# Optimization experiments

Hardware: AMD Instinct MI355X
Metric: run time of the kernel (lower is better)

The kernel has to match this reference:

```python
import math
import jax, jax.numpy as jnp
import numpy as np

B, S, D, H, DH = 4, 1024, 768, 24, 64  # batch, seq, d_model, n_heads (12*2), d_head
DG = 1  # d_gate


def setup_inputs() -> dict:
    key = jax.random.key(0)
    ks = jax.random.split(key, 12)
    sc = 0.02
    return {
        "x": jax.random.normal(ks[0], (B, S, D), dtype=jnp.float32),
        "W_Q": jax.random.normal(ks[1], (H, D, DH), dtype=jnp.float32) * sc,
        "W_K": jax.random.normal(ks[2], (H, D, DH), dtype=jnp.float32) * sc,
        "W_V": jax.random.normal(ks[3], (H, D, DH), dtype=jnp.float32) * sc,
        "W_O": jax.random.normal(ks[4], (H, DH, D), dtype=jnp.float32) * sc,
        "b_Q": jax.random.normal(ks[5], (H, DH), dtype=jnp.float32) * sc,
        "b_K": jax.random.normal(ks[6], (H, DH), dtype=jnp.float32) * sc,
        "b_V": jax.random.normal(ks[7], (H, DH), dtype=jnp.float32) * sc,
        "W_gate_Q": jax.random.normal(ks[8], (H, D, DG), dtype=jnp.float32) * sc,
        "W_gate_K": jax.random.normal(ks[9], (H, D, DG), dtype=jnp.float32) * sc,
        "b_gate_Q": jnp.zeros((H, DG), dtype=jnp.float32),
        "b_gate_K": jnp.zeros((H, DG), dtype=jnp.float32),
    }


def reference(x, W_Q, W_K, W_V, W_O, b_Q, b_K, b_V,
              W_gate_Q, W_gate_K, b_gate_Q, b_gate_K):
    eps = 1e-12
    # F.normalize: L2 over d_model axis (dim=1 of W_V, dim=2 of W_O)
    W_Vn = W_V / jnp.maximum(jnp.linalg.norm(W_V, axis=1, keepdims=True), eps)
    W_On = W_O / jnp.maximum(jnp.linalg.norm(W_O, axis=2, keepdims=True), eps)

    q = jnp.einsum('hmd,bqm->bqhd', W_Q, x) + b_Q            # [B,S,H,DH]
    k = jnp.einsum('hmd,bkm->bkhd', W_K, x) + b_K
    v = jnp.einsum('hmd,bkm->bkhd', W_Vn, x) + b_V
    qg = jnp.einsum('hmg,bqm->bqhg', W_gate_Q, x) + b_gate_Q  # [B,S,H,1]
    kg = jnp.einsum('hmg,bkm->bkhg', W_gate_K, x) + b_gate_K

    scores = jnp.einsum('bqhd,bkhd->bhqk', q, k)              # [B,H,S,S]
    gate = jnp.clip(jnp.einsum('bqhg,bkhg->bhqk', qg, kg), 0.0, 1.0)

    scaled = scores / math.sqrt(DH)
    causal = jnp.triu(jnp.ones((S, S), dtype=bool), 1)        # True above diagonal
    masked = jnp.where(causal[None, None], -jnp.inf, scaled)
    attn = jax.nn.softmax(masked, axis=-1)

    gated = gate * attn                                       # [B,H,S,S]
    # pre_z.sum(3) in the original == direct contraction over pos_k
    z = jnp.einsum('bhqk,bkhd->bhqd', gated, v)               # [B,H,S,DH]
    out = jnp.einsum('bhqd,hdm->bqm', z, W_On)                # sum over heads fused
    return out
```

## Files before the change

### kernel.cpp

```cpp
#include <hip/hip_runtime.h>
#include <math.h>


namespace {

typedef short bf16x8 __attribute__((ext_vector_type(8)));
typedef short bf16x4 __attribute__((ext_vector_type(4)));
typedef float f32x4 __attribute__((ext_vector_type(4)));
typedef unsigned short u16;
typedef u16 u16x8 __attribute__((ext_vector_type(8)));
typedef unsigned int u32;

constexpr int BB = 4, SS = 1024, DD = 768, HH = 24;
constexpr int RR = BB * SS;
constexpr int NC = HH * 64;
constexpr int NQKV = 3 * NC;
constexpr int NTOT = NQKV + 128;

__device__ inline u16 f2bf(float f) {
    u32 u = __float_as_uint(f);
    u += 0x7FFFu + ((u >> 16) & 1u);
    return (u16)(u >> 16);
}

__device__ __forceinline__ void async16(const void* g, const void* lds) {
    __builtin_amdgcn_global_load_lds(
        (const __attribute__((address_space(1))) u32*)(unsigned long long)(size_t)g,
        (__attribute__((address_space(3))) u32*)(u32)(size_t)lds, 16, 0, 0);
}

__global__ __launch_bounds__(256)
void norms_kernel(const float* __restrict__ Wv, const float* __restrict__ Wo,
                  float* __restrict__ invV, float* __restrict__ invO) {
    int j = blockIdx.x;
    int h = j >> 6, dh = j & 63;
    __shared__ float sv[256], so[256];
    float av = 0.f, ao = 0.f;
    for (int d = threadIdx.x; d < DD; d += 256) {
        float a = Wv[(h * DD + d) * 64 + dh];
        av += a * a;
        float b = Wo[(size_t)j * DD + d];
        ao += b * b;
    }
    sv[threadIdx.x] = av; so[threadIdx.x] = ao;
    __syncthreads();
    for (int s = 128; s > 0; s >>= 1) {
        if (threadIdx.x < s) {
            sv[threadIdx.x] += sv[threadIdx.x + s];
            so[threadIdx.x] += so[threadIdx.x + s];
        }
        __syncthreads();
    }
    if (threadIdx.x == 0) {
        invV[j] = 1.f / fmaxf(sqrtf(sv[0]), 1e-12f);
        invO[j] = 1.f / fmaxf(sqrtf(so[0]), 1e-12f);
    }
}

__global__ __launch_bounds__(256)
void x2bf_kernel(const float* __restrict__ x, u16* __restrict__ xb) {
    int idx = blockIdx.x * 256 + threadIdx.x;
    float4 v = ((const float4*)x)[idx];
    ushort4 o;
    o.x = f2bf(v.x); o.y = f2bf(v.y); o.z = f2bf(v.z); o.w = f2bf(v.w);
    ((ushort4*)xb)[idx] = o;
}

__global__ __launch_bounds__(256)
void pack_wqkv_kernel(const float* __restrict__ Wq, const float* __restrict__ Wk,
                      const float* __restrict__ Wv, const float* __restrict__ invV,
                      u16* __restrict__ wT) {
    const int k0 = blockIdx.x * 64, h = blockIdx.y, p = blockIdx.z;
    const float* W = (p == 0 ? Wq : p == 1 ? Wk : Wv) + (size_t)h * DD * 64;
    __shared__ float sT[64][68];
    const int t = threadIdx.x;
#pragma unroll
    for (int rep = 0; rep < 4; rep++) {
        int idx = t + rep * 256; int kk = idx >> 4, c = idx & 15;
        *(float4*)&sT[kk][c * 4] = *(const float4*)&W[(size_t)(k0 + kk) * 64 + c * 4];
    }
    __syncthreads();
#pragma unroll
    for (int rep = 0; rep < 2; rep++) {
        int idx = t + rep * 256; int dh = idx >> 3, cj = idx & 7;
        float sc = (p == 2) ? invV[h * 64 + dh] : 1.f;
        u16x8 o;
#pragma unroll
        for (int i = 0; i < 8; i++) o[i] = f2bf(sT[cj * 8 + i][dh] * sc);
        *(u16x8*)&wT[(size_t)(p * NC + h * 64 + dh) * DD + k0 + cj * 8] = o;
    }
}

__global__ __launch_bounds__(256)
void pack_gates_kernel(const float* __restrict__ Wgq, const float* __restrict__ Wgk,
                       u16* __restrict__ wT) {
    int g = blockIdx.x;
    u16* dst = wT + (size_t)(NQKV + g) * DD;
    if (g < 48) {
        const float* src = ((g & 1) ? Wgk : Wgq) + (size_t)(g >> 1) * DD;
        for (int c = threadIdx.x; c < DD; c += 256) dst[c] = f2bf(src[c]);
    } else {
        for (int c = threadIdx.x; c < DD; c += 256) dst[c] = 0;
    }
}

__global__ void pack_bias_kernel(const float* __restrict__ bq, const float* __restrict__ bk,
                                 const float* __restrict__ bv, float* __restrict__ biasp) {
    int n = blockIdx.x * 256 + threadIdx.x;
    if (n >= NQKV) return;
    int p = n / NC, rem = n % NC;
    biasp[n] = (p == 0) ? bq[rem] : (p == 1) ? bk[rem] : bv[rem];
}

__global__ __launch_bounds__(256)
void pack_wo_kernel(const float* __restrict__ Wo, u16* __restrict__ woT) {
    const int j0 = blockIdx.x * 64, d0 = blockIdx.y * 64;
    __shared__ float sT[64][68];
    const int t = threadIdx.x;
#pragma unroll
    for (int rep = 0; rep < 4; rep++) {
        int idx = t + rep * 256; int jj = idx >> 4, c = idx & 15;
        *(float4*)&sT[jj][c * 4] = *(const float4*)&Wo[(size_t)(j0 + jj) * DD + d0 + c * 4];
    }
    __syncthreads();
#pragma unroll
    for (int rep = 0; rep < 2; rep++) {
        int idx = t + rep * 256; int dd = idx >> 3, cj = idx & 7;
        u16x8 o;
#pragma unroll
        for (int i = 0; i < 8; i++) o[i] = f2bf(sT[cj * 8 + i][dd]);
        *(u16x8*)&woT[(size_t)(d0 + dd) * NC + j0 + cj * 8] = o;
    }
}

__global__ __launch_bounds__(256)
void qkv_gemm_kernel(const u16* __restrict__ xb, const u16* __restrict__ wT,
                     const float* __restrict__ biasp,
                     const float* __restrict__ bgq, const float* __restrict__ bgk,
                     u16* __restrict__ qo, u16* __restrict__ ko, u16* __restrict__ vto,
                     float* __restrict__ qgo, float* __restrict__ kgo) {
    const int flat = blockIdx.x + 37 * blockIdx.y;
    const int grp = flat / 296;
    const int rem = flat - grp * 296;
    const int row0 = (grp * 8 + (rem & 7)) * 128;
    const int n0 = (rem >> 3) * 128;
    const int t = threadIdx.x, w = t >> 6, l = t & 63, lr = l & 15, lq = l >> 4;
    const int wr = (w >> 1) * 64, wc = (w & 1) * 64;
    __shared__ u16 smem[4 * 4608];
    u16* sA = smem;
    u16* sB = smem + 8192;

    const int src_row = l >> 3;
    const int cbs = (l & 7) ^ src_row;
    const int swz = lr & 7;

    f32x4 acc[4][4] = {};
    for (int k0 = 0; k0 < DD; k0 += 64) {
        __syncthreads();
#pragma unroll
        for (int i = 0; i < 4; i++) {
            int ch = w * 4 + i;
            int rowA = ch * 8 + src_row;
            async16(xb + (size_t)(row0 + rowA) * DD + k0 + cbs * 8, sA + ch * 512);
            async16(wT + (size_t)(n0 + rowA) * DD + k0 + cbs * 8, sB + ch * 512);
        }
        __syncthreads();
#pragma unroll
        for (int s = 0; s < 2; s++) {
            const int j8 = ((s * 4 + lq) ^ swz) * 8;
            bf16x8 af[4], bf[4];
#pragma unroll
            for (int i = 0; i < 4; i++) {
                af[i] = *(const bf16x8*)&sA[(wr + i * 16 + lr) * 64 + j8];
                bf[i] = *(const bf16x8*)&sB[(wc + i * 16 + lr) * 64 + j8];
            }
#pragma unroll
            for (int mt = 0; mt < 4; mt++)
#pragma unroll
                for (int nt = 0; nt < 4; nt++)
                    acc[mt][nt] = __builtin_amdgcn_mfma_f32_16x16x32_bf16(
                        af[mt], bf[nt], acc[mt][nt], 0, 0, 0);
        }
    }
    __syncthreads();

    const int p = n0 / NC;
    const int b = row0 >> 10, s0 = row0 & (SS - 1);

    if (p == 3) {
        if (wc == 0) {
#pragma unroll
            for (int nt = 0; nt < 3; nt++) {
                int j = nt * 16 + lr, hh = j >> 1;
                float bias = (j & 1) ? bgk[hh] : bgq[hh];
                float* dst = (j & 1) ? kgo : qgo;
#pragma unroll
                for (int mt = 0; mt < 4; mt++)
#pragma unroll
                    for (int r = 0; r < 4; r++)
                        dst[((size_t)b * HH + hh) * SS + s0 + wr + mt * 16 + lq * 4 + r] =
                            acc[mt][nt][r] + bias;
            }
        }
        return;
    }

    const int cq = n0 + wc, srow = s0 + wr;
    u16* tw = smem + w * 4608;
    float bb[4];
#pragma unroll
    for (int nt = 0; nt < 4; nt++) bb[nt] = biasp[cq + nt * 16 + lr];

    if (p < 2) {
        const float sc = (p == 0) ? 0.18033688f : 1.f;
#pragma unroll
        for (int mt = 0; mt < 4; mt++)
#pragma unroll
            for (int nt = 0; nt < 4; nt++)
#pragma unroll
                for (int r = 0; r < 4; r++)
                    tw[(mt * 16 + lq * 4 + r) * 72 + nt * 16 + lr] =
                        f2bf((acc[mt][nt][r] + bb[nt]) * sc);
        const int h = (cq - p * NC) >> 6;
        u16* dst = (p == 0 ? qo : ko) + ((size_t)(b * HH + h) * SS + srow) * 64;
#pragma unroll
        for (int c = 0; c < 8; c++)
            *(u16x8*)&dst[(size_t)l * 64 + c * 8] = *(const u16x8*)&tw[l * 72 + c * 8];
    } else {
#pragma unroll
        for (int mt = 0; mt < 4; mt++)
#pragma unroll
            for (int nt = 0; nt < 4; nt++)
#pragma unroll
                for (int r = 0; r < 4; r++)
                    tw[(nt * 16 + lr) * 72 + mt * 16 + lq * 4 + r] =
                        f2bf(acc[mt][nt][r] + bb[nt]);
        const int h = (cq - 2 * NC) >> 6;
        u16* dst = vto + ((size_t)(b * HH + h) * 64 + l) * SS + srow;
#pragma unroll
        for (int c = 0; c < 8; c++)
            *(u16x8*)&dst[c * 8] = *(const u16x8*)&tw[l * 72 + c * 8];
    }
}

__global__ __launch_bounds__(256)
void attn_kernel(const u16* __restrict__ qb, const u16* __restrict__ kb,
                 const u16* __restrict__ vtb, const float* __restrict__ qg,
                 const float* __restrict__ kg, const float* __restrict__ invO,
                 u16* __restrict__ z) {
    const int h = blockIdx.x, b = blockIdx.y, pr = blockIdx.z;
    const int t = threadIdx.x, w = t >> 6, l = t & 63, lr = l & 15, lq = l >> 4;

    __shared__ u16 sK[2][64 * 64], sVT[2][64 * 64];

    const size_t bh = (size_t)(b * HH + h);
    const u16* Kb = kb + bh * SS * 64;
    const u16* Vt = vtb + bh * 64 * SS;
    const float* kgb = kg + bh * SS;

    const int src_row = l >> 3;
    const int cbs = (l & 7) ^ src_row;
    const int swz = lr & 7;

    auto stage = [&](int kt, int buf) {
#pragma unroll
        for (int i = 0; i < 2; i++) {
            int kc = w * 2 + i;
            int row = kc * 8 + src_row;
            async16(Kb + ((size_t)(kt * 64 + row)) * 64 + cbs * 8, sK[buf] + kc * 512);
            async16(Vt + (size_t)row * SS + kt * 64 + cbs * 8, sVT[buf] + kc * 512);
        }
    };

    stage(0, 0);
    int cur = 0;
#pragma unroll
    for (int sub = 0; sub < 2; sub++) {
        const int QT = sub ? (15 - pr) : pr;
        const int q0 = QT * 64 + w * 16;
        const u16* Qw = qb + (bh * SS + q0) * 64;
        bf16x8 aq0 = *(const bf16x8*)(Qw + (size_t)lr * 64 + lq * 8);
        bf16x8 aq1 = *(const bf16x8*)(Qw + (size_t)lr * 64 + 32 + lq * 8);
        const float qgr = qg[bh * SS + q0 + lr];

        f32x4 o[4] = {};
        float lacc = 0.f;

        for (int kt = 0; kt <= QT; kt++) {
            __syncthreads();
            if (kt < QT) stage(kt + 1, cur ^ 1);
            else if (sub == 0) stage(0, cur ^ 1);
            const u16* K_ = sK[cur];
            const u16* V_ = sVT[cur];

            float4 kgv[4];
#pragma unroll
            for (int nt = 0; nt < 4; nt++)
                kgv[nt] = *(const float4*)&kgb[kt * 64 + nt * 16 + lq * 4];

            f32x4 st[4] = {};
#pragma unroll
            for (int s = 0; s < 2; s++) {
                const int j8 = ((s * 4 + lq) ^ swz) * 8;
                const bf16x8 aqs = s ? aq1 : aq0;
#pragma unroll
                for (int nt = 0; nt < 4; nt++) {
                    bf16x8 bk = *(const bf16x8*)&K_[(nt * 16 + lr) * 64 + j8];
                    st[nt] = __builtin_amdgcn_mfma_f32_16x16x32_bf16(bk, aqs, st[nt], 0, 0, 0);
                }
            }

            const bool diag = (kt == QT);
            bf16x4 af[4];
#pragma unroll
            for (int nt = 0; nt < 4; nt++) {
#pragma unroll
                for (int r = 0; r < 4; r++) {
                    float pv = exp2f(st[nt][r]);
                    if (diag && (nt * 16 + lq * 4 + r > w * 16 + lr)) pv = 0.f;
                    lacc += pv;
                    float g = fminf(fmaxf(qgr * ((const float*)&kgv[nt])[r], 0.f), 1.f);
                    af[nt][r] = (short)f2bf(pv * g);
                }
            }

#pragma unroll
            for (int nt = 0; nt < 4; nt++) {
                const int vcol = (((nt * 2 + (lq >> 1)) ^ swz) << 3) + ((lq & 1) << 2);
#pragma unroll
                for (int dt = 0; dt < 4; dt++) {
                    bf16x4 vf = *(const bf16x4*)&V_[(dt * 16 + lr) * 64 + vcol];
                    o[dt] = __builtin_amdgcn_mfma_f32_16x16x16bf16_1k(af[nt], vf, o[dt], 0, 0, 0);
                }
            }
            cur ^= 1;
        }

        float lv = lacc;
        lv += __shfl_xor(lv, 16);
        lv += __shfl_xor(lv, 32);
        const float linv = __builtin_amdgcn_rcpf(lv);
        float inv_r[4];
#pragma unroll
        for (int r = 0; r < 4; r++)
            inv_r[r] = __shfl(linv, (l & 48) | (lq * 4 + r));

        const int col0 = h * 64;
#pragma unroll
        for (int dt = 0; dt < 4; dt++) {
            float io = invO[col0 + dt * 16 + lr];
#pragma unroll
            for (int r = 0; r < 4; r++) {
                float val = o[dt][r] * inv_r[r] * io;
                z[((size_t)b * SS + q0 + lq * 4 + r) * NC + col0 + dt * 16 + lr] = f2bf(val);
            }
        }
    }
}

__global__ __launch_bounds__(256)
void out_gemm_kernel(const u16* __restrict__ zb, const u16* __restrict__ woT,
                     float* __restrict__ out) {
    const int n0 = blockIdx.x * 64, row0 = blockIdx.y * 64;
    const int t = threadIdx.x, w = t >> 6, l = t & 63, lr = l & 15, lq = l >> 4;
    const int wr = (w >> 1) * 32, wc = (w & 1) * 32;
    __shared__ u16 sA[2][64 * 64], sB[2][64 * 64];

    const int src_row = l >> 3;
    const int cbs = (l & 7) ^ src_row;
    const int swz = lr & 7;

    auto stage = [&](int k0, int buf) {
#pragma unroll
        for (int i = 0; i < 2; i++) {
            int ch = w * 2 + i;
            int row = ch * 8 + src_row;
            async16(zb + (size_t)(row0 + row) * NC + k0 + cbs * 8, sA[buf] + ch * 512);
            async16(woT + (size_t)(n0 + row) * NC + k0 + cbs * 8, sB[buf] + ch * 512);
        }
    };

    stage(0, 0);
    int cur = 0;
    f32x4 acc[2][2] = {};
    for (int k0 = 0; k0 < NC; k0 += 64) {
        __syncthreads();
        if (k0 + 64 < NC) stage(k0 + 64, cur ^ 1);
#pragma unroll
        for (int s = 0; s < 2; s++) {
            const int j8 = ((s * 4 + lq) ^ swz) * 8;
            bf16x8 af[2], bf[2];
#pragma unroll
            for (int i = 0; i < 2; i++) {
                af[i] = *(const bf16x8*)&sA[cur][(wr + i * 16 + lr) * 64 + j8];
                bf[i] = *(const bf16x8*)&sB[cur][(wc + i * 16 + lr) * 64 + j8];
            }
#pragma unroll
            for (int mt = 0; mt < 2; mt++)
#pragma unroll
                for (int nt = 0; nt < 2; nt++)
                    acc[mt][nt] = __builtin_amdgcn_mfma_f32_16x16x32_bf16(
                        af[mt], bf[nt], acc[mt][nt], 0, 0, 0);
        }
        cur ^= 1;
    }
#pragma unroll
    for (int mt = 0; mt < 2; mt++)
#pragma unroll
        for (int nt = 0; nt < 2; nt++)
#pragma unroll
            for (int r = 0; r < 4; r++)
                out[(size_t)(row0 + wr + mt * 16 + lq * 4 + r) * DD + n0 + wc + nt * 16 + lr] =
                    acc[mt][nt][r];
}

}

extern "C" void kernel_launch(void* const* d_in, const int* in_sizes, int n_in,
                              void* d_out, int out_size, void* d_ws, size_t ws_size,
                              hipStream_t stream) {
    const float* x   = (const float*)d_in[0];
    const float* W_Q = (const float*)d_in[1];
    const float* W_K = (const float*)d_in[2];
    const float* W_V = (const float*)d_in[3];
    const float* W_O = (const float*)d_in[4];
    const float* b_Q = (const float*)d_in[5];
    const float* b_K = (const float*)d_in[6];
    const float* b_V = (const float*)d_in[7];
    const float* Wgq = (const float*)d_in[8];
    const float* Wgk = (const float*)d_in[9];
    const float* bgq = (const float*)d_in[10];
    const float* bgk = (const float*)d_in[11];
    float* out = (float*)d_out;

    char* wsb = (char*)d_ws;
    auto alloc = [&](size_t bytes) -> char* {
        char* p = wsb;
        wsb += (bytes + 255) & ~(size_t)255;
        return p;
    };
    float* invV  = (float*)alloc((size_t)NC * 4);
    float* invO  = (float*)alloc((size_t)NC * 4);
    float* biasp = (float*)alloc((size_t)NQKV * 4);
    float* qg    = (float*)alloc((size_t)RR * HH * 4);
    float* kg    = (float*)alloc((size_t)RR * HH * 4);
    u16* xb      = (u16*)alloc((size_t)RR * DD * 2);
    u16* wT      = (u16*)alloc((size_t)NTOT * DD * 2);
    u16* woT     = (u16*)alloc((size_t)DD * NC * 2);
    u16* qb      = (u16*)alloc((size_t)RR * 64 * HH * 2);
    u16* kb      = (u16*)alloc((size_t)RR * 64 * HH * 2);
    u16* vtb     = (u16*)alloc((size_t)RR * 64 * HH * 2);
    u16* zb      = (u16*)alloc((size_t)RR * NC * 2);

    norms_kernel<<<NC, 256, 0, stream>>>(W_V, W_O, invV, invO);
    x2bf_kernel<<<RR * DD / 4 / 256, 256, 0, stream>>>(x, xb);
    pack_wqkv_kernel<<<dim3(DD / 64, HH, 3), 256, 0, stream>>>(W_Q, W_K, W_V, invV, wT);
    pack_gates_kernel<<<128, 256, 0, stream>>>(Wgq, Wgk, wT);
    pack_bias_kernel<<<(NQKV + 255) / 256, 256, 0, stream>>>(b_Q, b_K, b_V, biasp);
    pack_wo_kernel<<<dim3(NC / 64, DD / 64), 256, 0, stream>>>(W_O, woT);
    qkv_gemm_kernel<<<dim3(NTOT / 128, RR / 128), 256, 0, stream>>>(
        xb, wT, biasp, bgq, bgk, qb, kb, vtb, qg, kg);
    attn_kernel<<<dim3(HH, BB, 8), 256, 0, stream>>>(
        qb, kb, vtb, qg, kg, invO, zb);
    out_gemm_kernel<<<dim3(DD / 64, RR / 64), 256, 0, stream>>>(zb, woT, out);
}
```

Measured before the change: 233.2 us.

## Process 128-row query tiles per attention block and drop bias pack kernel

Attention blocks now each own one 128-query tile, with every wave computing 32 query rows (two 16-row MFMA tiles). This replaces the old pairing of two 64-row tiles, so each staged K/V chunk and its LDS fragment reads feed twice as many MFMAs, and heaviest tiles are launched first. Separately, the pack_bias kernel is removed and the QKV GEMM reads b_Q/b_K/b_V directly, saving one launch. The tradeoff is that blocks now differ widely in work (1 to 16 K tiles) instead of being balanced, register pressure rises, and waves whose rows are fully masked idle through early iterations.

```diff
diff --git a/kernel.cpp b/kernel.cpp
--- a/kernel.cpp
+++ b/kernel.cpp
@@ -104,14 +104,6 @@
     }
 }
 
-__global__ void pack_bias_kernel(const float* __restrict__ bq, const float* __restrict__ bk,
-                                 const float* __restrict__ bv, float* __restrict__ biasp) {
-    int n = blockIdx.x * 256 + threadIdx.x;
-    if (n >= NQKV) return;
-    int p = n / NC, rem = n % NC;
-    biasp[n] = (p == 0) ? bq[rem] : (p == 1) ? bk[rem] : bv[rem];
-}
-
 __global__ __launch_bounds__(256)
 void pack_wo_kernel(const float* __restrict__ Wo, u16* __restrict__ woT) {
     const int j0 = blockIdx.x * 64, d0 = blockIdx.y * 64;
@@ -135,7 +127,8 @@
 
 __global__ __launch_bounds__(256)
 void qkv_gemm_kernel(const u16* __restrict__ xb, const u16* __restrict__ wT,
-                     const float* __restrict__ biasp,
+                     const float* __restrict__ bq, const float* __restrict__ bk,
+                     const float* __restrict__ bv,
                      const float* __restrict__ bgq, const float* __restrict__ bgk,
                      u16* __restrict__ qo, u16* __restrict__ ko, u16* __restrict__ vto,
                      float* __restrict__ qgo, float* __restrict__ kgo) {
@@ -207,9 +200,10 @@
 
     const int cq = n0 + wc, srow = s0 + wr;
     u16* tw = smem + w * 4608;
+    const float* bias = (p == 0) ? bq : (p == 1) ? bk : bv;
     float bb[4];
 #pragma unroll
-    for (int nt = 0; nt < 4; nt++) bb[nt] = biasp[cq + nt * 16 + lr];
+    for (int nt = 0; nt < 4; nt++) bb[nt] = bias[cq - p * NC + nt * 16 + lr];
 
     if (p < 2) {
         const float sc = (p == 0) ? 0.18033688f : 1.f;
@@ -248,7 +242,8 @@
                  const u16* __restrict__ vtb, const float* __restrict__ qg,
                  const float* __restrict__ kg, const float* __restrict__ invO,
                  u16* __restrict__ z) {
-    const int h = blockIdx.x, b = blockIdx.y, pr = blockIdx.z;
+    const int h = blockIdx.x, b = blockIdx.y;
+    const int tile = 7 - blockIdx.z;
     const int t = threadIdx.x, w = t >> 6, l = t & 63, lr = l & 15, lq = l >> 4;
 
     __shared__ u16 sK[2][64 * 64], sVT[2][64 * 64];
@@ -272,55 +267,67 @@
         }
     };
 
+    const int q0w = tile * 128 + w * 32;
+    const u16* Qw = qb + (bh * SS + q0w) * 64;
+    bf16x8 aq[2][2];
+#pragma unroll
+    for (int qi = 0; qi < 2; qi++)
+#pragma unroll
+        for (int s = 0; s < 2; s++)
+            aq[qi][s] = *(const bf16x8*)(Qw + (size_t)(qi * 16 + lr) * 64 + s * 32 + lq * 8);
+    float qgr[2];
+#pragma unroll
+    for (int qi = 0; qi < 2; qi++) qgr[qi] = qg[bh * SS + q0w + qi * 16 + lr];
+
+    f32x4 o[2][4] = {};
+    float lacc[2] = {0.f, 0.f};
+
+    const int ktmax = 2 * tile + 1;
     stage(0, 0);
     int cur = 0;
-#pragma unroll
-    for (int sub = 0; sub < 2; sub++) {
-        const int QT = sub ? (15 - pr) : pr;
-        const int q0 = QT * 64 + w * 16;
-        const u16* Qw = qb + (bh * SS + q0) * 64;
-        bf16x8 aq0 = *(const bf16x8*)(Qw + (size_t)lr * 64 + lq * 8);
-        bf16x8 aq1 = *(const bf16x8*)(Qw + (size_t)lr * 64 + 32 + lq * 8);
-        const float qgr = qg[bh * SS + q0 + lr];
-
-        f32x4 o[4] = {};
-        float lacc = 0.f;
-
-        for (int kt = 0; kt <= QT; kt++) {
-            __syncthreads();
-            if (kt < QT) stage(kt + 1, cur ^ 1);
-            else if (sub == 0) stage(0, cur ^ 1);
-            const u16* K_ = sK[cur];
-            const u16* V_ = sVT[cur];
-
+    for (int kt = 0; kt <= ktmax; kt++) {
+        __syncthreads();
+        if (kt < ktmax) stage(kt + 1, cur ^ 1);
+        const u16* K_ = sK[cur];
+        const u16* V_ = sVT[cur];
+
+        if (kt * 64 < q0w + 32) {
             float4 kgv[4];
 #pragma unroll
             for (int nt = 0; nt < 4; nt++)
                 kgv[nt] = *(const float4*)&kgb[kt * 64 + nt * 16 + lq * 4];
 
-            f32x4 st[4] = {};
+            f32x4 st[2][4] = {};
 #pragma unroll
             for (int s = 0; s < 2; s++) {
                 const int j8 = ((s * 4 + lq) ^ swz) * 8;
-                const bf16x8 aqs = s ? aq1 : aq0;
 #pragma unroll
                 for (int nt = 0; nt < 4; nt++) {
                     bf16x8 bk = *(const bf16x8*)&K_[(nt * 16 + lr) * 64 + j8];
-                    st[nt] = __builtin_amdgcn_mfma_f32_16x16x32_bf16(bk, aqs, st[nt], 0, 0, 0);
+#pragma unroll
+                    for (int qi = 0; qi < 2; qi++)
+                        st[qi][nt] = __builtin_amdgcn_mfma_f32_16x16x32_bf16(
+                            bk, aq[qi][s], st[qi][nt], 0, 0, 0);
                 }
             }
 
-            const bool diag = (kt == QT);
-            bf16x4 af[4];
-#pragma unroll
-            for (int nt = 0; nt < 4; nt++) {
-#pragma unroll
-                for (int r = 0; r < 4; r++) {
-                    float pv = exp2f(st[nt][r]);
-                    if (diag && (nt * 16 + lq * 4 + r > w * 16 + lr)) pv = 0.f;
-                    lacc += pv;
-                    float g = fminf(fmaxf(qgr * ((const float*)&kgv[nt])[r], 0.f), 1.f);
-                    af[nt][r] = (short)f2bf(pv * g);
+            bf16x4 af[2][4];
+#pragma unroll
+            for (int qi = 0; qi < 2; qi++) {
+                const bool need_mask = (kt * 64 + 63 > q0w + qi * 16);
+#pragma unroll
+                for (int nt = 0; nt < 4; nt++) {
+#pragma unroll
+                    for (int r = 0; r < 4; r++) {
+                        float pv = exp2f(st[qi][nt][r]);
+                        if (need_mask &&
+                            (kt * 64 + nt * 16 + lq * 4 + r > q0w + qi * 16 + lr))
+                            pv = 0.f;
+                        lacc[qi] += pv;
+                        float g = fminf(fmaxf(qgr[qi] * ((const float*)&kgv[nt])[r],
+                                              0.f), 1.f);
+                        af[qi][nt][r] = (short)f2bf(pv * g);
+                    }
                 }
             }
 
@@ -330,13 +337,20 @@
 #pragma unroll
                 for (int dt = 0; dt < 4; dt++) {
                     bf16x4 vf = *(const bf16x4*)&V_[(dt * 16 + lr) * 64 + vcol];
-                    o[dt] = __builtin_amdgcn_mfma_f32_16x16x16bf16_1k(af[nt], vf, o[dt], 0, 0, 0);
+#pragma unroll
+                    for (int qi = 0; qi < 2; qi++)
+                        o[qi][dt] = __builtin_amdgcn_mfma_f32_16x16x16bf16_1k(
+                            af[qi][nt], vf, o[qi][dt], 0, 0, 0);
                 }
             }
-            cur ^= 1;
-        }
-
-        float lv = lacc;
+        }
+        cur ^= 1;
+    }
+
+    const int col0 = h * 64;
+#pragma unroll
+    for (int qi = 0; qi < 2; qi++) {
+        float lv = lacc[qi];
         lv += __shfl_xor(lv, 16);
         lv += __shfl_xor(lv, 32);
         const float linv = __builtin_amdgcn_rcpf(lv);
@@ -344,15 +358,14 @@
 #pragma unroll
         for (int r = 0; r < 4; r++)
             inv_r[r] = __shfl(linv, (l & 48) | (lq * 4 + r));
-
-        const int col0 = h * 64;
 #pragma unroll
         for (int dt = 0; dt < 4; dt++) {
             float io = invO[col0 + dt * 16 + lr];
 #pragma unroll
             for (int r = 0; r < 4; r++) {
-                float val = o[dt][r] * inv_r[r] * io;
-                z[((size_t)b * SS + q0 + lq * 4 + r) * NC + col0 + dt * 16 + lr] = f2bf(val);
+                float val = o[qi][dt][r] * inv_r[r] * io;
+                z[((size_t)b * SS + q0w + qi * 16 + lq * 4 + r) * NC + col0 + dt * 16 + lr] =
+                    f2bf(val);
             }
         }
     }
@@ -441,7 +454,6 @@
     };
     float* invV  = (float*)alloc((size_t)NC * 4);
     float* invO  = (float*)alloc((size_t)NC * 4);
-    float* biasp = (float*)alloc((size_t)NQKV * 4);
     float* qg    = (float*)alloc((size_t)RR * HH * 4);
     float* kg    = (float*)alloc((size_t)RR * HH * 4);
     u16* xb      = (u16*)alloc((size_t)RR * DD * 2);
@@ -456,10 +468,9 @@
     x2bf_kernel<<<RR * DD / 4 / 256, 256, 0, stream>>>(x, xb);
     pack_wqkv_kernel<<<dim3(DD / 64, HH, 3), 256, 0, stream>>>(W_Q, W_K, W_V, invV, wT);
     pack_gates_kernel<<<128, 256, 0, stream>>>(Wgq, Wgk, wT);
-    pack_bias_kernel<<<(NQKV + 255) / 256, 256, 0, stream>>>(b_Q, b_K, b_V, biasp);
     pack_wo_kernel<<<dim3(NC / 64, DD / 64), 256, 0, stream>>>(W_O, woT);
     qkv_gemm_kernel<<<dim3(NTOT / 128, RR / 128), 256, 0, stream>>>(
-        xb, wT, biasp, bgq, bgk, qb, kb, vtb, qg, kg);
+        xb, wT, b_Q, b_K, b_V, bgq, bgk, qb, kb, vtb, qg, kg);
     attn_kernel<<<dim3(HH, BB, 8), 256, 0, stream>>>(
         qb, kb, vtb, qg, kg, invO, zb);
     out_gemm_kernel<<<dim3(DD / 64, RR / 64), 256, 0, stream>>>(zb, woT, out);
```

Measured after the change: 231.6 us. About the same (-0.7%).
